# Kernel tuning notes

Measured on AMD Instinct MI355X. Metric: run time of the kernel, lower is better.

The kernel has to match this reference:

```python
import jax, jax.numpy as jnp
import numpy as np

B, T, D, A = 8, 256, 512, 512  # hidden dim D must equal attn size A per the TF code


def setup_inputs() -> dict:
    key = jax.random.key(0)
    ks = jax.random.split(key, 12)
    g = lambda k, shp, fan: jax.random.normal(k, shp, jnp.float32) * (1.0 / np.sqrt(fan))
    return {
        "state_outputs": jax.random.normal(ks[0], (B, T, D), jnp.float32),
        "final_state": jax.random.normal(ks[1], (B, D), jnp.float32),
        "intent_v": g(ks[2], (A,), A),
        "W_ih": g(ks[3], (D, A), D), "b_ih": jnp.zeros((A,), jnp.float32),
        "W_ii": g(ks[4], (D, A), D), "b_ii": jnp.zeros((A,), jnp.float32),
        "slot_v": g(ks[5], (A,), A),
        "W_sh": g(ks[6], (D, A), D), "b_sh": jnp.zeros((A,), jnp.float32),
        "W_si": g(ks[7], (D, A), D), "b_si": jnp.zeros((A,), jnp.float32),
    }


def reference(state_outputs, final_state, intent_v, W_ih, b_ih, W_ii, b_ii,
              slot_v, W_sh, b_sh, W_si, b_si):
    # ---- intent attention ----
    ih = jnp.einsum('btd,da->bta', state_outputs, W_ih) + b_ih        # [B,T,A]
    ii = final_state @ W_ii + b_ii                                     # [B,A]
    intent_score = jnp.sum(intent_v * jnp.tanh(ih + ii[:, None, :]), axis=-1)  # [B,T]
    intent_w = jax.nn.softmax(intent_score, axis=-1)
    c_intent = jnp.einsum('bt,btd->bd', intent_w, state_outputs)       # [B,D]

    # ---- slot attention ----
    sh = jnp.einsum('btd,da->bta', state_outputs, W_sh) + b_sh         # keys   [B,T,A]
    si = jnp.einsum('btd,da->bta', state_outputs, W_si) + b_si         # queries[B,T,A]
    # score[b,t,s] over pairs: tanh(sh[b,s] + si[b,t]) . slot_v
    slot_score = jnp.sum(slot_v * jnp.tanh(sh[:, None, :, :] + si[:, :, None, :]), axis=-1)  # [B,T,T]
    slot_w = jax.nn.softmax(slot_score, axis=-1)
    c_slot = jnp.einsum('bts,bsd->btd', slot_w, state_outputs)         # [B,T,D]
    return c_slot, c_intent
```

## Files before the change

kernel.cpp:

```cpp
#include <hip/hip_runtime.h>

#define BB 8
#define TT 256
#define DD 512
#define AA 512

#define PS 2.8853900817779268f
#define LOG2E 1.4426950408889634f

typedef __attribute__((ext_vector_type(8))) short short8;
typedef __attribute__((ext_vector_type(4))) float f32x4;

__device__ __forceinline__ float fast_tanh(float x) {
    float e = __builtin_amdgcn_exp2f(x * PS);
    float r = __builtin_amdgcn_rcpf(1.0f + e);
    return fmaf(-2.0f, r, 1.0f);
}

__device__ __forceinline__ ushort f2bf(float x) {
    uint u = __float_as_uint(x);
    uint r = (u + 0x7fffu + ((u >> 16) & 1u)) >> 16;
    return (ushort)r;
}
__device__ __forceinline__ float bf2f(ushort h) {
    return __uint_as_float(((uint)h) << 16);
}

#define ABYTE(k0) (((k0) < 1024 ? (k0) : (k0) - 1024) * 2)
#define BBYTE(k0) (((k0) < 512 ? (k0) : (k0) - 512) * 2)

__global__ __launch_bounds__(256) void prep(const float* __restrict__ SO,
                                            ushort* __restrict__ Ast,
                                            const float* __restrict__ Wsh,
                                            const float* __restrict__ Wsi,
                                            const float* __restrict__ Wih,
                                            ushort* __restrict__ Wt,
                                            const float* __restrict__ fs_g,
                                            const float* __restrict__ Wii,
                                            const float* __restrict__ bii,
                                            float* __restrict__ ii) {
    const int bid = blockIdx.x;
    const int tid = threadIdx.x;
    __shared__ float T[32][33];
    __shared__ float fs[DD];

    if (bid < 16) {
        int b = bid >> 1, half = bid & 1;
        int a = half * 256 + tid;
        fs[tid]       = fs_g[b * DD + tid];
        fs[tid + 256] = fs_g[b * DD + tid + 256];
        __syncthreads();
        float acc = bii[a];
        #pragma unroll 8
        for (int d = 0; d < DD; ++d)
            acc = fmaf(fs[d], Wii[(size_t)d * AA + a], acc);
        ii[b * AA + a] = acc;
    } else if (bid < 784) {
        int lbid = bid - 16;
        int z = lbid >> 8;
        int rem = lbid & 255;
        const float* W = (z == 0) ? Wsh : (z == 1) ? Wsi : Wih;
        int k0 = (rem & 15) * 32, n0 = (rem >> 4) * 32;
        int tx = tid & 31, ty = tid >> 5;
        #pragma unroll
        for (int r = 0; r < 4; ++r) {
            int kl = ty * 4 + r;
            T[kl][tx] = W[(size_t)(k0 + kl) * 512 + n0 + tx];
        }
        __syncthreads();
        size_t nbase = (size_t)z * 512 + n0;
        #pragma unroll
        for (int r = 0; r < 4; ++r) {
            int nl = ty * 4 + r;
            float v = T[tx][nl];
            ushort hi = f2bf(v);
            ushort lo = f2bf(v - bf2f(hi));
            Wt[(nbase + nl) * 1024 + k0 + tx]       = hi;
            Wt[(nbase + nl) * 1024 + 512 + k0 + tx] = lo;
        }
    } else {
        int qid = (bid - 784) * 256 + tid;
        int m = qid >> 7;
        int k4 = (qid & 127) * 4;
        float4 v = *reinterpret_cast<const float4*>(&SO[(size_t)m * 512 + k4]);
        ushort4 hi, lo;
        hi.x = f2bf(v.x); lo.x = f2bf(v.x - bf2f(hi.x));
        hi.y = f2bf(v.y); lo.y = f2bf(v.y - bf2f(hi.y));
        hi.z = f2bf(v.z); lo.z = f2bf(v.z - bf2f(hi.z));
        hi.w = f2bf(v.w); lo.w = f2bf(v.w - bf2f(hi.w));
        *reinterpret_cast<ushort4*>(&Ast[(size_t)m * 1024 + k4])       = hi;
        *reinterpret_cast<ushort4*>(&Ast[(size_t)m * 1024 + 512 + k4]) = lo;
    }
}

__global__ __launch_bounds__(256) void gemm_mfma(
    const ushort* __restrict__ Ast, const ushort* __restrict__ Wt,
    const float* __restrict__ bsh, const float* __restrict__ bsi,
    const float* __restrict__ bih,
    const float* __restrict__ ii, const float* __restrict__ iv,
    float* __restrict__ EhT, float* __restrict__ Es, float* __restrict__ ipart) {
    __shared__ __align__(16) ushort Al[2][64 * 64];
    __shared__ __align__(16) ushort Bl[2][64 * 64];
    const int tid = threadIdx.x;
    const int wave = tid >> 6, lane = tid & 63;
    const int wr = wave >> 1, wc = wave & 1;
    const int m0 = blockIdx.x * 64;
    const int by = blockIdx.y;
    const int n0 = by * 64;
    const int l15 = lane & 15, kb = lane >> 4;

    f32x4 acc[2][2] = {};

    const char* Ab = reinterpret_cast<const char*>(Ast);
    const char* Bb = reinterpret_cast<const char*>(Wt);
    char* AlB = reinterpret_cast<char*>(&Al[0][0]);
    char* BlB = reinterpret_cast<char*>(&Bl[0][0]);

    const int srow = tid >> 2, sslot = tid & 3;
    const int lw0 = srow * 128 + (((sslot    ) ^ (srow & 7)) * 16);
    const int lw1 = srow * 128 + (((sslot + 4) ^ (srow & 7)) * 16);
    const char* agp = Ab + (size_t)(m0 + srow) * 2048 + sslot * 16;
    const char* bgp = Bb + (size_t)(n0 + srow) * 2048 + sslot * 16;

    int aro[2][2], bro[2][2];
    #pragma unroll
    for (int i = 0; i < 2; ++i) {
        int ra = wr * 32 + i * 16 + l15;
        int rb = wc * 32 + i * 16 + l15;
        #pragma unroll
        for (int kk = 0; kk < 2; ++kk) {
            aro[kk][i] = ra * 128 + (((kk * 4 + kb) ^ (ra & 7)) * 16);
            bro[kk][i] = rb * 128 + (((kk * 4 + kb) ^ (rb & 7)) * 16);
        }
    }

    {
        short8 a0 = *reinterpret_cast<const short8*>(agp + ABYTE(0));
        short8 a1 = *reinterpret_cast<const short8*>(agp + ABYTE(0) + 64);
        short8 b0 = *reinterpret_cast<const short8*>(bgp + BBYTE(0));
        short8 b1 = *reinterpret_cast<const short8*>(bgp + BBYTE(0) + 64);
        *reinterpret_cast<short8*>(AlB + lw0) = a0;
        *reinterpret_cast<short8*>(AlB + lw1) = a1;
        *reinterpret_cast<short8*>(BlB + lw0) = b0;
        *reinterpret_cast<short8*>(BlB + lw1) = b1;
    }
    __syncthreads();

    int cur = 0;
    for (int it = 0; it < 24; ++it) {
        short8 pa0, pa1, pb0, pb1;
        const bool pf = (it + 1 < 24);
        if (pf) {
            int k0 = (it + 1) * 64;
            int ab = ABYTE(k0), bb = BBYTE(k0);
            pa0 = *reinterpret_cast<const short8*>(agp + ab);
            pa1 = *reinterpret_cast<const short8*>(agp + ab + 64);
            pb0 = *reinterpret_cast<const short8*>(bgp + bb);
            pb1 = *reinterpret_cast<const short8*>(bgp + bb + 64);
        }
        const char* Ac = AlB + cur * 8192;
        const char* Bc = BlB + cur * 8192;
        #pragma unroll
        for (int kk = 0; kk < 2; ++kk) {
            short8 af[2], bf[2];
            #pragma unroll
            for (int i = 0; i < 2; ++i) {
                af[i] = *reinterpret_cast<const short8*>(Ac + aro[kk][i]);
                bf[i] = *reinterpret_cast<const short8*>(Bc + bro[kk][i]);
            }
            #pragma unroll
            for (int i = 0; i < 2; ++i)
                #pragma unroll
                for (int j = 0; j < 2; ++j)
                    acc[i][j] = __builtin_amdgcn_mfma_f32_16x16x32_bf16(
                        af[i], bf[j], acc[i][j], 0, 0, 0);
        }
        if (pf) {
            char* An = AlB + (cur ^ 1) * 8192;
            char* Bn = BlB + (cur ^ 1) * 8192;
            *reinterpret_cast<short8*>(An + lw0) = pa0;
            *reinterpret_cast<short8*>(An + lw1) = pa1;
            *reinterpret_cast<short8*>(Bn + lw0) = pb0;
            *reinterpret_cast<short8*>(Bn + lw1) = pb1;
        }
        __syncthreads();
        cur ^= 1;
    }

    const int b = m0 >> 8;
    if (by < 8) {
        #pragma unroll
        for (int i = 0; i < 2; ++i) {
            int t0 = (m0 & 255) + wr * 32 + i * 16 + kb * 4;
            #pragma unroll
            for (int j = 0; j < 2; ++j) {
                int n = n0 + wc * 32 + j * 16 + l15;
                float bbv = bsh[n];
                float4 v;
                v.x = __builtin_amdgcn_exp2f((acc[i][j][0] + bbv) * PS);
                v.y = __builtin_amdgcn_exp2f((acc[i][j][1] + bbv) * PS);
                v.z = __builtin_amdgcn_exp2f((acc[i][j][2] + bbv) * PS);
                v.w = __builtin_amdgcn_exp2f((acc[i][j][3] + bbv) * PS);
                *reinterpret_cast<float4*>(&EhT[((size_t)b * 512 + n) * 256 + t0]) = v;
            }
        }
    } else if (by < 16) {
        #pragma unroll
        for (int i = 0; i < 2; ++i) {
            #pragma unroll
            for (int j = 0; j < 2; ++j) {
                int n = n0 - 512 + wc * 32 + j * 16 + l15;
                float bbv = bsi[n];
                #pragma unroll
                for (int r = 0; r < 4; ++r) {
                    int m = m0 + wr * 32 + i * 16 + kb * 4 + r;
                    Es[(size_t)m * 512 + n] = __builtin_amdgcn_exp2f((acc[i][j][r] + bbv) * PS);
                }
            }
        }
    } else {
        int slot = (by - 16) * 2 + wc;
        #pragma unroll
        for (int i = 0; i < 2; ++i) {
            float p0 = 0.f, p1 = 0.f, p2 = 0.f, p3 = 0.f;
            #pragma unroll
            for (int j = 0; j < 2; ++j) {
                int n = n0 - 1024 + wc * 32 + j * 16 + l15;
                float add = bih[n] + ii[b * 512 + n];
                float w = iv[n];
                p0 = fmaf(w, fast_tanh(acc[i][j][0] + add), p0);
                p1 = fmaf(w, fast_tanh(acc[i][j][1] + add), p1);
                p2 = fmaf(w, fast_tanh(acc[i][j][2] + add), p2);
                p3 = fmaf(w, fast_tanh(acc[i][j][3] + add), p3);
            }
            #pragma unroll
            for (int off = 1; off < 16; off <<= 1) {
                p0 += __shfl_xor(p0, off);
                p1 += __shfl_xor(p1, off);
                p2 += __shfl_xor(p2, off);
                p3 += __shfl_xor(p3, off);
            }
            int mb = m0 + wr * 32 + i * 16 + kb * 4;
            if (l15 == 0) ipart[slot * 2048 + mb + 0] = p0;
            if (l15 == 1) ipart[slot * 2048 + mb + 1] = p1;
            if (l15 == 2) ipart[slot * 2048 + mb + 2] = p2;
            if (l15 == 3) ipart[slot * 2048 + mb + 3] = p3;
        }
    }
}

#define TS 64
#define KS 16
#define LPAD 72

__global__ __launch_bounds__(256) void k0_ii(const float* __restrict__ fs_g,
                                             const float* __restrict__ Wii,
                                             const float* __restrict__ bii,
                                             float* __restrict__ ii) {
    int b = blockIdx.x, tid = threadIdx.x;
    int a = blockIdx.y * 256 + tid;
    __shared__ float fs[DD];
    fs[tid]       = fs_g[b * DD + tid];
    fs[tid + 256] = fs_g[b * DD + tid + 256];
    __syncthreads();
    float acc = bii[a];
    #pragma unroll 8
    for (int d = 0; d < DD; ++d)
        acc = fmaf(fs[d], Wii[(size_t)d * AA + a], acc);
    ii[b * AA + a] = acc;
}

__global__ __launch_bounds__(256) void k1_gemm_old(
    const float* __restrict__ SO,
    const float* __restrict__ Wsh, const float* __restrict__ bsh,
    const float* __restrict__ Wsi, const float* __restrict__ bsi,
    const float* __restrict__ Wih, const float* __restrict__ bih,
    const float* __restrict__ ii, const float* __restrict__ iv,
    float* __restrict__ EhT, float* __restrict__ Es, float* __restrict__ ipart) {
    const int mode = blockIdx.z;
    const float* W;
    const float* bias;
    if (mode == 0)      { W = Wsh; bias = bsh; }
    else if (mode == 1) { W = Wsi; bias = bsi; }
    else                { W = Wih; bias = bih; }

    const int m0 = blockIdx.x * TS;
    const int n0 = blockIdx.y * TS;
    const int tid = threadIdx.x;
    const int tx = tid & 15, ty = tid >> 4;

    __shared__ __align__(16) float As[KS][LPAD];
    __shared__ __align__(16) float Bs[KS][LPAD];
    __shared__ __align__(16) float Cs[TS][LPAD];

    float acc[4][4] = {};
    const int arow = tid >> 2;
    const int akc  = (tid & 3) * 4;
    const int brw  = tid >> 4;
    const int bnc  = (tid & 15) * 4;

    for (int k0 = 0; k0 < DD; k0 += KS) {
        float4 av = *reinterpret_cast<const float4*>(&SO[(m0 + arow) * DD + k0 + akc]);
        As[akc + 0][arow] = av.x;
        As[akc + 1][arow] = av.y;
        As[akc + 2][arow] = av.z;
        As[akc + 3][arow] = av.w;
        float4 bv = *reinterpret_cast<const float4*>(&W[(k0 + brw) * AA + n0 + bnc]);
        *reinterpret_cast<float4*>(&Bs[brw][bnc]) = bv;
        __syncthreads();
        #pragma unroll
        for (int kk = 0; kk < KS; ++kk) {
            float4 a4 = *reinterpret_cast<const float4*>(&As[kk][ty * 4]);
            float4 b4 = *reinterpret_cast<const float4*>(&Bs[kk][tx * 4]);
            float av_[4] = {a4.x, a4.y, a4.z, a4.w};
            float bv_[4] = {b4.x, b4.y, b4.z, b4.w};
            #pragma unroll
            for (int i = 0; i < 4; ++i)
                #pragma unroll
                for (int j = 0; j < 4; ++j)
                    acc[i][j] = fmaf(av_[i], bv_[j], acc[i][j]);
        }
        __syncthreads();
    }

    if (mode == 1) {
        #pragma unroll
        for (int i = 0; i < 4; ++i) {
            int m = m0 + ty * 4 + i;
            float4 v;
            v.x = __builtin_amdgcn_exp2f((acc[i][0] + bias[n0 + tx * 4 + 0]) * PS);
            v.y = __builtin_amdgcn_exp2f((acc[i][1] + bias[n0 + tx * 4 + 1]) * PS);
            v.z = __builtin_amdgcn_exp2f((acc[i][2] + bias[n0 + tx * 4 + 2]) * PS);
            v.w = __builtin_amdgcn_exp2f((acc[i][3] + bias[n0 + tx * 4 + 3]) * PS);
            *reinterpret_cast<float4*>(&Es[(size_t)m * AA + n0 + tx * 4]) = v;
        }
    } else if (mode == 0) {
        #pragma unroll
        for (int i = 0; i < 4; ++i)
            #pragma unroll
            for (int j = 0; j < 4; ++j)
                Cs[tx * 4 + j][ty * 4 + i] =
                    __builtin_amdgcn_exp2f((acc[i][j] + bias[n0 + tx * 4 + j]) * PS);
        __syncthreads();
        int row = tid >> 2, part = tid & 3;
        int bb = m0 >> 8;
        int tstart = (m0 & 255) + part * 16;
        float* dst = &EhT[bb * (AA * TT) + (n0 + row) * TT + tstart];
        #pragma unroll
        for (int q = 0; q < 4; ++q) {
            float4 v = *reinterpret_cast<const float4*>(&Cs[row][part * 16 + q * 4]);
            *reinterpret_cast<float4*>(&dst[q * 4]) = v;
        }
    } else {
        int bb = m0 >> 8;
        #pragma unroll
        for (int i = 0; i < 4; ++i) {
            float p = 0.f;
            #pragma unroll
            for (int j = 0; j < 4; ++j) {
                int n = n0 + tx * 4 + j;
                float x = acc[i][j] + bias[n] + ii[bb * AA + n];
                p = fmaf(iv[n], fast_tanh(x), p);
            }
            Cs[ty * 4 + i][tx] = p;
        }
        __syncthreads();
        if (tid < 64) {
            float s = 0.f;
            #pragma unroll
            for (int k = 0; k < 16; ++k) s += Cs[tid][k];
            ipart[blockIdx.y * 2048 + m0 + tid] = s;
        }
    }
}

__global__ __launch_bounds__(512) void k3_fused(const float* __restrict__ SO,
                                                const float* __restrict__ EhT,
                                                const float* __restrict__ Es,
                                                const float* __restrict__ sv_g,
                                                const float* __restrict__ ipart,
                                                float* __restrict__ out_cslot,
                                                float* __restrict__ out_cint,
                                                int npart) {
    const int bid = blockIdx.x;
    const int tid = threadIdx.x;

    __shared__ __align__(16) float est[512][4];
    __shared__ __align__(16) float sv[512];
    __shared__ __align__(8)  float yp[4][4][256];
    __shared__ __align__(16) float wlt[256][4];
    __shared__ float redm[4][2];
    __shared__ float reds[4][2];
    __shared__ float redI[256];
    __shared__ float wlI[256];

    const int b = bid & 7;
    const int t0 = (bid >> 3) * 4;
    const int sp = tid & 127;
    const int ah = tid >> 7;
    const int abase = ah * 128;

    {
        const float* esrc = &Es[(size_t)(b * 256 + t0) * 512];
        #pragma unroll
        for (int i = tid; i < 2048; i += 512) est[i & 511][i >> 9] = esrc[i];
        sv[tid] = sv_g[tid];
    }
    __syncthreads();

    const float* hp = &EhT[((size_t)b * 512 + abase) * 256 + 2 * sp];
    float a00=0.f,a01=0.f,a10=0.f,a11=0.f,a20=0.f,a21=0.f,a30=0.f,a31=0.f;
    float2 h0[4], h1[4];
    #pragma unroll
    for (int u = 0; u < 4; ++u)
        h0[u] = *reinterpret_cast<const float2*>(&hp[u * 256]);

    #define SCORE4(A0, H) do {                                                         \
        float4 v4 = *reinterpret_cast<const float4*>(&sv[abase + (A0)]);               \
        _Pragma("unroll")                                                              \
        for (int u = 0; u < 4; ++u) {                                                  \
            float4 e4 = *reinterpret_cast<const float4*>(&est[abase + (A0) + u][0]);   \
            float vv = (u == 0) ? v4.x : (u == 1) ? v4.y : (u == 2) ? v4.z : v4.w;     \
            float hx = H[u].x, hy = H[u].y;                                            \
            a00 = fmaf(vv, __builtin_amdgcn_rcpf(fmaf(hx, e4.x, 1.f)), a00);           \
            a01 = fmaf(vv, __builtin_amdgcn_rcpf(fmaf(hy, e4.x, 1.f)), a01);           \
            a10 = fmaf(vv, __builtin_amdgcn_rcpf(fmaf(hx, e4.y, 1.f)), a10);           \
            a11 = fmaf(vv, __builtin_amdgcn_rcpf(fmaf(hy, e4.y, 1.f)), a11);           \
            a20 = fmaf(vv, __builtin_amdgcn_rcpf(fmaf(hx, e4.z, 1.f)), a20);           \
            a21 = fmaf(vv, __builtin_amdgcn_rcpf(fmaf(hy, e4.z, 1.f)), a21);           \
            a30 = fmaf(vv, __builtin_amdgcn_rcpf(fmaf(hx, e4.w, 1.f)), a30);           \
            a31 = fmaf(vv, __builtin_amdgcn_rcpf(fmaf(hy, e4.w, 1.f)), a31);           \
        }                                                                              \
    } while (0)

    for (int a0 = 0; a0 < 128; a0 += 8) {
        #pragma unroll
        for (int u = 0; u < 4; ++u)
            h1[u] = *reinterpret_cast<const float2*>(&hp[(a0 + 4 + u) * 256]);
        SCORE4(a0, h0);
        #pragma unroll
        for (int u = 0; u < 4; ++u)
            h0[u] = *reinterpret_cast<const float2*>(&hp[(a0 + 8 + u) * 256]);
        SCORE4(a0 + 4, h1);
    }

    *reinterpret_cast<float2*>(&yp[ah][0][2 * sp]) = make_float2(a00, a01);
    *reinterpret_cast<float2*>(&yp[ah][1][2 * sp]) = make_float2(a10, a11);
    *reinterpret_cast<float2*>(&yp[ah][2][2 * sp]) = make_float2(a20, a21);
    *reinterpret_cast<float2*>(&yp[ah][3][2 * sp]) = make_float2(a30, a31);
    __syncthreads();

    {
        const int g = ah;
        const int L = sp;
        const int w2 = (tid >> 6) & 1;
        float yL = (yp[0][g][L]       + yp[1][g][L])       + (yp[2][g][L]       + yp[3][g][L]);
        float yH = (yp[0][g][L + 128] + yp[1][g][L + 128]) + (yp[2][g][L + 128] + yp[3][g][L + 128]);
        float mn = fminf(yL, yH);
        #pragma unroll
        for (int off = 1; off < 64; off <<= 1)
            mn = fminf(mn, __shfl_xor(mn, off));
        if ((tid & 63) == 0) redm[g][w2] = mn;
        __syncthreads();
        mn = fminf(redm[g][0], redm[g][1]);
        float eL = __builtin_amdgcn_exp2f(PS * (mn - yL));
        float eH = __builtin_amdgcn_exp2f(PS * (mn - yH));
        float sm = eL + eH;
        #pragma unroll
        for (int off = 1; off < 64; off <<= 1)
            sm += __shfl_xor(sm, off);
        if ((tid & 63) == 0) reds[g][w2] = sm;
        __syncthreads();
        sm = reds[g][0] + reds[g][1];
        float rs = __builtin_amdgcn_rcpf(sm);
        wlt[L][g]       = eL * rs;
        wlt[L + 128][g] = eH * rs;
    }
    __syncthreads();

    {
        const int d = tid;
        const float* sop = &SO[(size_t)b * 256 * 512 + d];
        float c0 = 0.f, c1 = 0.f, c2 = 0.f, c3 = 0.f;
        for (int s0 = 0; s0 < 256; s0 += 4) {
            float so[4];
            #pragma unroll
            for (int u = 0; u < 4; ++u) so[u] = sop[(s0 + u) * 512];
            #pragma unroll
            for (int u = 0; u < 4; ++u) {
                float4 w4 = *reinterpret_cast<const float4*>(&wlt[s0 + u][0]);
                c0 = fmaf(w4.x, so[u], c0);
                c1 = fmaf(w4.y, so[u], c1);
                c2 = fmaf(w4.z, so[u], c2);
                c3 = fmaf(w4.w, so[u], c3);
            }
        }
        float* op = &out_cslot[((size_t)(b * 256 + t0)) * 512 + d];
        op[0] = c0; op[512] = c1; op[1024] = c2; op[1536] = c3;
    }

    if (bid < 8) {
        __syncthreads();
        float sc = 0.f;
        if (tid < 256) {
            for (int nb = 0; nb < npart; ++nb) sc += ipart[nb * 2048 + b * 256 + tid];
            redI[tid] = sc;
        }
        __syncthreads();
        for (int off = 128; off > 0; off >>= 1) {
            if (tid < off) redI[tid] = fmaxf(redI[tid], redI[tid + off]);
            __syncthreads();
        }
        float mx = redI[0];
        __syncthreads();
        float e = 0.f;
        if (tid < 256) { e = __builtin_amdgcn_exp2f((sc - mx) * LOG2E); redI[tid] = e; }
        __syncthreads();
        for (int off = 128; off > 0; off >>= 1) {
            if (tid < off) redI[tid] += redI[tid + off];
            __syncthreads();
        }
        if (tid < 256) wlI[tid] = e * __builtin_amdgcn_rcpf(redI[0]);
        __syncthreads();
        const int d = tid;
        float c = 0.f;
        const float* sop = &SO[(size_t)b * 256 * 512 + d];
        for (int s0 = 0; s0 < 256; s0 += 4) {
            float so[4];
            #pragma unroll
            for (int u = 0; u < 4; ++u) so[u] = sop[(s0 + u) * 512];
            #pragma unroll
            for (int u = 0; u < 4; ++u) c = fmaf(wlI[s0 + u], so[u], c);
        }
        out_cint[(size_t)b * 512 + d] = c;
    }
}

extern "C" void kernel_launch(void* const* d_in, const int* in_sizes, int n_in,
                              void* d_out, int out_size, void* d_ws, size_t ws_size,
                              hipStream_t stream) {
    const float* SO  = (const float*)d_in[0];
    const float* FS  = (const float*)d_in[1];
    const float* IV  = (const float*)d_in[2];
    const float* Wih = (const float*)d_in[3];
    const float* bih = (const float*)d_in[4];
    const float* Wii = (const float*)d_in[5];
    const float* bii = (const float*)d_in[6];
    const float* SV  = (const float*)d_in[7];
    const float* Wsh = (const float*)d_in[8];
    const float* bsh = (const float*)d_in[9];
    const float* Wsi = (const float*)d_in[10];
    const float* bsi = (const float*)d_in[11];

    float* ws    = (float*)d_ws;
    float* EhT   = ws;
    float* Es    = ws + 1048576;
    float* ii    = ws + 2097152;
    float* ipart = ws + 2101248;
    ushort* Ast  = (ushort*)(ws + 2134016);
    ushort* Wt   = (ushort*)(ws + 3182592);
    const size_t NEED = (size_t)3969024 * 4;

    float* out_cslot = (float*)d_out;
    float* out_cint  = out_cslot + BB * TT * DD;

    if (ws_size >= NEED) {
        prep<<<1808, 256, 0, stream>>>(SO, Ast, Wsh, Wsi, Wih, Wt, FS, Wii, bii, ii);
        gemm_mfma<<<dim3(32, 24), 256, 0, stream>>>(Ast, Wt, bsh, bsi, bih, ii, IV,
                                                    EhT, Es, ipart);
        k3_fused<<<512, 512, 0, stream>>>(SO, EhT, Es, SV, ipart, out_cslot, out_cint, 16);
    } else {
        k0_ii<<<dim3(BB, 2), 256, 0, stream>>>(FS, Wii, bii, ii);
        k1_gemm_old<<<dim3(32, 8, 3), 256, 0, stream>>>(SO, Wsh, bsh, Wsi, bsi, Wih, bih,
                                                        ii, IV, EhT, Es, ipart);
        k3_fused<<<512, 512, 0, stream>>>(SO, EhT, Es, SV, ipart, out_cslot, out_cint, 8);
    }
}
```

Baseline: 93.33 us.

## Widen per-thread score tile to 4x4 and split A across eight waves

The slot-score loop in k3_fused now has each thread compute 4 keys × 4 queries (float4 loads of EhT) instead of 2 × 4, and splits the attention dimension into eight 64-wide slices instead of four 128-wide ones. The partial-score buffer grows to 8 slices and the reduction sums 8 partials per element. The softmax thread mapping is reindexed to match. The aim is to reuse each shared-memory est/sv load across more FMAs and to issue wider global loads, at the cost of more accumulator registers and a larger LDS buffer.

```diff
diff --git a/kernel.cpp b/kernel.cpp
--- a/kernel.cpp
+++ b/kernel.cpp
@@ -387,7 +387,7 @@
 
     __shared__ __align__(16) float est[512][4];
     __shared__ __align__(16) float sv[512];
-    __shared__ __align__(8)  float yp[4][4][256];
+    __shared__ __align__(16) float yp[8][4][256];
     __shared__ __align__(16) float wlt[256][4];
     __shared__ float redm[4][2];
     __shared__ float reds[4][2];
@@ -396,9 +396,9 @@
 
     const int b = bid & 7;
     const int t0 = (bid >> 3) * 4;
-    const int sp = tid & 127;
-    const int ah = tid >> 7;
-    const int abase = ah * 128;
+    const int sq = tid & 63;
+    const int ah = tid >> 6;
+    const int abase = ah * 64;
 
     {
         const float* esrc = &Es[(size_t)(b * 256 + t0) * 512];
@@ -408,12 +408,12 @@
     }
     __syncthreads();
 
-    const float* hp = &EhT[((size_t)b * 512 + abase) * 256 + 2 * sp];
-    float a00=0.f,a01=0.f,a10=0.f,a11=0.f,a20=0.f,a21=0.f,a30=0.f,a31=0.f;
-    float2 h0[4], h1[4];
+    const float* hp = &EhT[((size_t)b * 512 + abase) * 256 + 4 * sq];
+    float acc[4][4] = {};
+    float4 h0[4], h1[4];
     #pragma unroll
     for (int u = 0; u < 4; ++u)
-        h0[u] = *reinterpret_cast<const float2*>(&hp[u * 256]);
+        h0[u] = *reinterpret_cast<const float4*>(&hp[u * 256]);
 
     #define SCORE4(A0, H) do {                                                         \
         float4 v4 = *reinterpret_cast<const float4*>(&sv[abase + (A0)]);               \
@@ -421,60 +421,64 @@
         for (int u = 0; u < 4; ++u) {                                                  \
             float4 e4 = *reinterpret_cast<const float4*>(&est[abase + (A0) + u][0]);   \
             float vv = (u == 0) ? v4.x : (u == 1) ? v4.y : (u == 2) ? v4.z : v4.w;     \
-            float hx = H[u].x, hy = H[u].y;                                            \
-            a00 = fmaf(vv, __builtin_amdgcn_rcpf(fmaf(hx, e4.x, 1.f)), a00);           \
-            a01 = fmaf(vv, __builtin_amdgcn_rcpf(fmaf(hy, e4.x, 1.f)), a01);           \
-            a10 = fmaf(vv, __builtin_amdgcn_rcpf(fmaf(hx, e4.y, 1.f)), a10);           \
-            a11 = fmaf(vv, __builtin_amdgcn_rcpf(fmaf(hy, e4.y, 1.f)), a11);           \
-            a20 = fmaf(vv, __builtin_amdgcn_rcpf(fmaf(hx, e4.z, 1.f)), a20);           \
-            a21 = fmaf(vv, __builtin_amdgcn_rcpf(fmaf(hy, e4.z, 1.f)), a21);           \
-            a30 = fmaf(vv, __builtin_amdgcn_rcpf(fmaf(hx, e4.w, 1.f)), a30);           \
-            a31 = fmaf(vv, __builtin_amdgcn_rcpf(fmaf(hy, e4.w, 1.f)), a31);           \
+            float hx = H[u].x, hy = H[u].y, hz = H[u].z, hw = H[u].w;                  \
+            _Pragma("unroll")                                                          \
+            for (int t = 0; t < 4; ++t) {                                              \
+                float ee = (t == 0) ? e4.x : (t == 1) ? e4.y : (t == 2) ? e4.z : e4.w; \
+                acc[t][0] = fmaf(vv, __builtin_amdgcn_rcpf(fmaf(hx, ee, 1.f)), acc[t][0]); \
+                acc[t][1] = fmaf(vv, __builtin_amdgcn_rcpf(fmaf(hy, ee, 1.f)), acc[t][1]); \
+                acc[t][2] = fmaf(vv, __builtin_amdgcn_rcpf(fmaf(hz, ee, 1.f)), acc[t][2]); \
+                acc[t][3] = fmaf(vv, __builtin_amdgcn_rcpf(fmaf(hw, ee, 1.f)), acc[t][3]); \
+            }                                                                          \
         }                                                                              \
     } while (0)
 
-    for (int a0 = 0; a0 < 128; a0 += 8) {
+    for (int a0 = 0; a0 < 64; a0 += 8) {
         #pragma unroll
         for (int u = 0; u < 4; ++u)
-            h1[u] = *reinterpret_cast<const float2*>(&hp[(a0 + 4 + u) * 256]);
+            h1[u] = *reinterpret_cast<const float4*>(&hp[(a0 + 4 + u) * 256]);
         SCORE4(a0, h0);
         #pragma unroll
         for (int u = 0; u < 4; ++u)
-            h0[u] = *reinterpret_cast<const float2*>(&hp[(a0 + 8 + u) * 256]);
+            h0[u] = *reinterpret_cast<const float4*>(&hp[(a0 + 8 + u) * 256]);
         SCORE4(a0 + 4, h1);
     }
 
-    *reinterpret_cast<float2*>(&yp[ah][0][2 * sp]) = make_float2(a00, a01);
-    *reinterpret_cast<float2*>(&yp[ah][1][2 * sp]) = make_float2(a10, a11);
-    *reinterpret_cast<float2*>(&yp[ah][2][2 * sp]) = make_float2(a20, a21);
-    *reinterpret_cast<float2*>(&yp[ah][3][2 * sp]) = make_float2(a30, a31);
+    #pragma unroll
+    for (int t = 0; t < 4; ++t)
+        *reinterpret_cast<float4*>(&yp[ah][t][4 * sq]) =
+            make_float4(acc[t][0], acc[t][1], acc[t][2], acc[t][3]);
     __syncthreads();
 
     {
-        const int g = ah;
-        const int L = sp;
-        const int w2 = (tid >> 6) & 1;
-        float yL = (yp[0][g][L]       + yp[1][g][L])       + (yp[2][g][L]       + yp[3][g][L]);
-        float yH = (yp[0][g][L + 128] + yp[1][g][L + 128]) + (yp[2][g][L + 128] + yp[3][g][L + 128]);
+        const int q = ah & 3, hf = ah >> 2;
+        const int lane = tid & 63;
+        const int sL = hf * 128 + lane, sH = sL + 64;
+        float yL = 0.f, yH = 0.f;
+        #pragma unroll
+        for (int k = 0; k < 8; ++k) {
+            yL += yp[k][q][sL];
+            yH += yp[k][q][sH];
+        }
         float mn = fminf(yL, yH);
         #pragma unroll
         for (int off = 1; off < 64; off <<= 1)
             mn = fminf(mn, __shfl_xor(mn, off));
-        if ((tid & 63) == 0) redm[g][w2] = mn;
-        __syncthreads();
-        mn = fminf(redm[g][0], redm[g][1]);
+        if (lane == 0) redm[q][hf] = mn;
+        __syncthreads();
+        mn = fminf(redm[q][0], redm[q][1]);
         float eL = __builtin_amdgcn_exp2f(PS * (mn - yL));
         float eH = __builtin_amdgcn_exp2f(PS * (mn - yH));
         float sm = eL + eH;
         #pragma unroll
         for (int off = 1; off < 64; off <<= 1)
             sm += __shfl_xor(sm, off);
-        if ((tid & 63) == 0) reds[g][w2] = sm;
-        __syncthreads();
-        sm = reds[g][0] + reds[g][1];
+        if (lane == 0) reds[q][hf] = sm;
+        __syncthreads();
+        sm = reds[q][0] + reds[q][1];
         float rs = __builtin_amdgcn_rcpf(sm);
-        wlt[L][g]       = eL * rs;
-        wlt[L + 128][g] = eH * rs;
+        wlt[sL][q] = eL * rs;
+        wlt[sH][q] = eH * rs;
     }
     __syncthreads();
 
```

After: 105.9 us. 1.13x slower.

## Pair reciprocals in slot scoring and deepen GEMM global prefetch to two stages

Applied to the files above, without the earlier changes.

The slot score loop now combines two attention terms over a common denominator, computing va/d1 + vb/d2 as (va*d2 + vb*d1)/(d1*d2). This halves the number of rcp transcendental instructions at the cost of extra multiplies and FMAs, and carries some risk of overflow when the exp-based denominators are large. Separately, the projection GEMM loop is fully unrolled and issues global loads two iterations ahead into a pair of register buffers, to hide more global-memory latency at the cost of higher register pressure.

```diff
diff --git a/kernel.cpp b/kernel.cpp
--- a/kernel.cpp
+++ b/kernel.cpp
@@ -134,32 +134,35 @@
         }
     }
 
-    {
-        short8 a0 = *reinterpret_cast<const short8*>(agp + ABYTE(0));
-        short8 a1 = *reinterpret_cast<const short8*>(agp + ABYTE(0) + 64);
-        short8 b0 = *reinterpret_cast<const short8*>(bgp + BBYTE(0));
-        short8 b1 = *reinterpret_cast<const short8*>(bgp + BBYTE(0) + 64);
-        *reinterpret_cast<short8*>(AlB + lw0) = a0;
-        *reinterpret_cast<short8*>(AlB + lw1) = a1;
-        *reinterpret_cast<short8*>(BlB + lw0) = b0;
-        *reinterpret_cast<short8*>(BlB + lw1) = b1;
-    }
+    #define GLOAD4(H, S) do {                                        \
+        const int k0_ = (S) * 64;                                    \
+        const int ab_ = ABYTE(k0_), bb_ = BBYTE(k0_);                \
+        H[0] = *reinterpret_cast<const short8*>(agp + ab_);          \
+        H[1] = *reinterpret_cast<const short8*>(agp + ab_ + 64);     \
+        H[2] = *reinterpret_cast<const short8*>(bgp + bb_);          \
+        H[3] = *reinterpret_cast<const short8*>(bgp + bb_ + 64);     \
+    } while (0)
+
+    #define STLDS(BUF, H) do {                                       \
+        char* An_ = AlB + (BUF) * 8192;                              \
+        char* Bn_ = BlB + (BUF) * 8192;                              \
+        *reinterpret_cast<short8*>(An_ + lw0) = H[0];                \
+        *reinterpret_cast<short8*>(An_ + lw1) = H[1];                \
+        *reinterpret_cast<short8*>(Bn_ + lw0) = H[2];                \
+        *reinterpret_cast<short8*>(Bn_ + lw1) = H[3];                \
+    } while (0)
+
+    short8 hld[2][4];
+    GLOAD4(hld[0], 0);
+    STLDS(0, hld[0]);
+    GLOAD4(hld[1], 1);
     __syncthreads();
 
-    int cur = 0;
+    #pragma unroll
     for (int it = 0; it < 24; ++it) {
-        short8 pa0, pa1, pb0, pb1;
-        const bool pf = (it + 1 < 24);
-        if (pf) {
-            int k0 = (it + 1) * 64;
-            int ab = ABYTE(k0), bb = BBYTE(k0);
-            pa0 = *reinterpret_cast<const short8*>(agp + ab);
-            pa1 = *reinterpret_cast<const short8*>(agp + ab + 64);
-            pb0 = *reinterpret_cast<const short8*>(bgp + bb);
-            pb1 = *reinterpret_cast<const short8*>(bgp + bb + 64);
-        }
-        const char* Ac = AlB + cur * 8192;
-        const char* Bc = BlB + cur * 8192;
+        if (it + 2 < 24) GLOAD4(hld[it & 1], it + 2);
+        const char* Ac = AlB + (it & 1) * 8192;
+        const char* Bc = BlB + (it & 1) * 8192;
         #pragma unroll
         for (int kk = 0; kk < 2; ++kk) {
             short8 af[2], bf[2];
@@ -175,16 +178,8 @@
                     acc[i][j] = __builtin_amdgcn_mfma_f32_16x16x32_bf16(
                         af[i], bf[j], acc[i][j], 0, 0, 0);
         }
-        if (pf) {
-            char* An = AlB + (cur ^ 1) * 8192;
-            char* Bn = BlB + (cur ^ 1) * 8192;
-            *reinterpret_cast<short8*>(An + lw0) = pa0;
-            *reinterpret_cast<short8*>(An + lw1) = pa1;
-            *reinterpret_cast<short8*>(Bn + lw0) = pb0;
-            *reinterpret_cast<short8*>(Bn + lw1) = pb1;
-        }
-        __syncthreads();
-        cur ^= 1;
+        if (it + 1 < 24) STLDS((it + 1) & 1, hld[(it + 1) & 1]);
+        __syncthreads();
     }
 
     const int b = m0 >> 8;
@@ -415,33 +410,42 @@
     for (int u = 0; u < 4; ++u)
         h0[u] = *reinterpret_cast<const float2*>(&hp[u * 256]);
 
-    #define SCORE4(A0, H) do {                                                         \
-        float4 v4 = *reinterpret_cast<const float4*>(&sv[abase + (A0)]);               \
-        _Pragma("unroll")                                                              \
-        for (int u = 0; u < 4; ++u) {                                                  \
-            float4 e4 = *reinterpret_cast<const float4*>(&est[abase + (A0) + u][0]);   \
-            float vv = (u == 0) ? v4.x : (u == 1) ? v4.y : (u == 2) ? v4.z : v4.w;     \
-            float hx = H[u].x, hy = H[u].y;                                            \
-            a00 = fmaf(vv, __builtin_amdgcn_rcpf(fmaf(hx, e4.x, 1.f)), a00);           \
-            a01 = fmaf(vv, __builtin_amdgcn_rcpf(fmaf(hy, e4.x, 1.f)), a01);           \
-            a10 = fmaf(vv, __builtin_amdgcn_rcpf(fmaf(hx, e4.y, 1.f)), a10);           \
-            a11 = fmaf(vv, __builtin_amdgcn_rcpf(fmaf(hy, e4.y, 1.f)), a11);           \
-            a20 = fmaf(vv, __builtin_amdgcn_rcpf(fmaf(hx, e4.z, 1.f)), a20);           \
-            a21 = fmaf(vv, __builtin_amdgcn_rcpf(fmaf(hy, e4.z, 1.f)), a21);           \
-            a30 = fmaf(vv, __builtin_amdgcn_rcpf(fmaf(hx, e4.w, 1.f)), a30);           \
-            a31 = fmaf(vv, __builtin_amdgcn_rcpf(fmaf(hy, e4.w, 1.f)), a31);           \
-        }                                                                              \
+    #define PAIRT(HA, HB, E1, E2, VA, VB, ACC0, ACC1) do {                         \
+        float d1x = fmaf((HA).x, (E1), 1.f);                                       \
+        float d2x = fmaf((HB).x, (E2), 1.f);                                       \
+        ACC0 = fmaf(fmaf((VA), d2x, (VB) * d1x),                                   \
+                    __builtin_amdgcn_rcpf(d1x * d2x), ACC0);                       \
+        float d1y = fmaf((HA).y, (E1), 1.f);                                       \
+        float d2y = fmaf((HB).y, (E2), 1.f);                                       \
+        ACC1 = fmaf(fmaf((VA), d2y, (VB) * d1y),                                   \
+                    __builtin_amdgcn_rcpf(d1y * d2y), ACC1);                       \
+    } while (0)
+
+    #define SCOREP(A0, H) do {                                                     \
+        float4 v4 = *reinterpret_cast<const float4*>(&sv[abase + (A0)]);           \
+        float4 e0 = *reinterpret_cast<const float4*>(&est[abase + (A0) + 0][0]);   \
+        float4 e1 = *reinterpret_cast<const float4*>(&est[abase + (A0) + 1][0]);   \
+        float4 e2 = *reinterpret_cast<const float4*>(&est[abase + (A0) + 2][0]);   \
+        float4 e3 = *reinterpret_cast<const float4*>(&est[abase + (A0) + 3][0]);   \
+        PAIRT(H[0], H[1], e0.x, e1.x, v4.x, v4.y, a00, a01);                       \
+        PAIRT(H[0], H[1], e0.y, e1.y, v4.x, v4.y, a10, a11);                       \
+        PAIRT(H[0], H[1], e0.z, e1.z, v4.x, v4.y, a20, a21);                       \
+        PAIRT(H[0], H[1], e0.w, e1.w, v4.x, v4.y, a30, a31);                       \
+        PAIRT(H[2], H[3], e2.x, e3.x, v4.z, v4.w, a00, a01);                       \
+        PAIRT(H[2], H[3], e2.y, e3.y, v4.z, v4.w, a10, a11);                       \
+        PAIRT(H[2], H[3], e2.z, e3.z, v4.z, v4.w, a20, a21);                       \
+        PAIRT(H[2], H[3], e2.w, e3.w, v4.z, v4.w, a30, a31);                       \
     } while (0)
 
     for (int a0 = 0; a0 < 128; a0 += 8) {
         #pragma unroll
         for (int u = 0; u < 4; ++u)
             h1[u] = *reinterpret_cast<const float2*>(&hp[(a0 + 4 + u) * 256]);
-        SCORE4(a0, h0);
+        SCOREP(a0, h0);
         #pragma unroll
         for (int u = 0; u < 4; ++u)
             h0[u] = *reinterpret_cast<const float2*>(&hp[(a0 + 8 + u) * 256]);
-        SCORE4(a0 + 4, h1);
+        SCOREP(a0 + 4, h1);
     }
 
     *reinterpret_cast<float2*>(&yp[ah][0][2 * sp]) = make_float2(a00, a01);
```

New measurement: 90.96 us. 1.03x faster.
